# Performance work log

Measured on AMD Instinct MI355X. Metric: run time of the kernel, lower is better.

The kernel has to match this reference:

```python
import jax, jax.numpy as jnp
import numpy as np

U, I, K = 20000, 10000, 64
HID = [128, 64, 32, 16]  # hidden[0] must equal 2*K
B = 4096


def _lin(key, out_f, in_f):
    # torch nn.Linear default init ~ U(-1/sqrt(in), 1/sqrt(in)); normal/sqrt(in) is fine for a baseline
    return jax.random.normal(key, (out_f, in_f), jnp.float32) / np.sqrt(in_f)


def setup_inputs() -> dict:
    key = jax.random.key(0)
    ks = jax.random.split(key, 12)
    # near-binary implicit-feedback interaction matrix [U+1, I+1]
    interactions = (jax.random.uniform(ks[0], (U + 1, I + 1)) < 0.05).astype(jnp.float32)
    user_idx = jax.random.randint(ks[1], (B,), 0, U)
    item_idx = jax.random.randint(ks[2], (B,), 0, I)
    W_u = _lin(ks[3], K, I)   # proj_u: Linear(n_items -> K, bias=False)
    W_i = _lin(ks[4], K, U)   # proj_i: Linear(n_users -> K, bias=False)
    inp = dict(interactions=interactions, user_idx=user_idx, item_idx=item_idx,
               W_u=W_u, W_i=W_i)
    # matching_fn: 3 blocks of Linear + LayerNorm (+ReLU, dropout=0 in eval)
    for j in range(1, len(HID)):
        inp[f'W{j}'] = _lin(ks[4 + j], HID[j], HID[j - 1])
        inp[f'b{j}'] = jnp.zeros((HID[j],), jnp.float32)
        inp[f'g{j}'] = jnp.ones((HID[j],), jnp.float32)
        inp[f'be{j}'] = jnp.zeros((HID[j],), jnp.float32)
    inp['Wp'] = _lin(ks[8], 1, HID[-1])
    inp['bp'] = jnp.zeros((1,), jnp.float32)
    return inp


def _layernorm(x, g, b, eps=1e-5):
    m = jnp.mean(x, axis=-1, keepdims=True)
    v = jnp.mean(jnp.square(x - m), axis=-1, keepdims=True)
    return (x - m) * jax.lax.rsqrt(v + eps) * g + b


def reference(interactions, user_idx, item_idx, W_u, W_i,
              W1, b1, g1, be1, W2, b2, g2, be2, W3, b3, g3, be3, Wp, bp):
    rows = jnp.arange(user_idx.shape[0])
    # gather user history rows [B, I], zero-mask the target item
    u_slice = interactions[user_idx, :-1].at[rows, item_idx].set(0.0)
    # gather item history rows [B, U], zero-mask the target user
    i_slice = interactions.T[item_idx, :-1].at[rows, user_idx].set(0.0)
    u_emb = u_slice @ W_u.T  # [B, K]
    i_emb = i_slice @ W_i.T  # [B, K]
    x = jnp.concatenate([u_emb, i_emb], axis=-1)  # [B, 2K]
    for (W, b, g, be) in ((W1, b1, g1, be1), (W2, b2, g2, be2), (W3, b3, g3, be3)):
        x = jax.nn.relu(_layernorm(x @ W.T + b, g, be))
    logit = jnp.squeeze(x @ Wp.T + bp, -1)  # [B]
    return logit
```

## Files before the change

### kernel.cpp

```cpp
#include <hip/hip_runtime.h>

#define U_ROWS 20000
#define I_COLS 10000
#define LDI    10001
#define B_N    4096
#define SC     625
#define NPAN_C 79
#define NC_C   8
#define SUT    79
#define NP_U   8
#define SPU_T  10
#define SU_P   316
#define ABP    10240
#define ABRP   1280

typedef __attribute__((ext_vector_type(8))) __bf16 bf16x8;
typedef __attribute__((ext_vector_type(4))) float f32x4;

__device__ __forceinline__ unsigned short f2bf(float f) {
    unsigned int u = __float_as_uint(f);
    return (unsigned short)((u + 0x7FFFu + ((u >> 16) & 1u)) >> 16);
}

__device__ __forceinline__ bf16x8 expand8(unsigned int byte) {
    union { unsigned int i[4]; bf16x8 v; } af;
#pragma unroll
    for (int q = 0; q < 4; ++q) {
        unsigned int lo = (byte & (1u << (2 * q)))     ? 0x00003F80u : 0u;
        unsigned int hi = (byte & (1u << (2 * q + 1))) ? 0x3F800000u : 0u;
        af.i[q] = lo | hi;
    }
    return af.v;
}

__global__ __launch_bounds__(256) void k_bitize(
    const float* __restrict__ A,
    unsigned int* __restrict__ Abit, unsigned char* __restrict__ Abr,
    const float* __restrict__ Wu, const float* __restrict__ Wi,
    unsigned short* __restrict__ Pu, unsigned short* __restrict__ Pi,
    const float* __restrict__ W1, const float* __restrict__ W2, const float* __restrict__ W3,
    float* __restrict__ Wt1, float* __restrict__ Wt2, float* __restrict__ Wt3,
    float* __restrict__ WuT, float* __restrict__ WiT)
{
    const int t = threadIdx.x;
    if ((int)blockIdx.x < SC) {
        const int s = blockIdx.x;
        unsigned int wq[5][8];
#pragma unroll
        for (int q = 0; q < 5; ++q)
#pragma unroll
            for (int j = 0; j < 8; ++j) wq[q][j] = 0u;

        for (int r = 0; r < 32; ++r) {
            const float* row = A + (size_t)(s * 32 + r) * LDI;
#pragma unroll
            for (int q = 0; q < 5; ++q) {
                const int c0 = 8 * t + 2048 * q;
                f32x4 a0 = *(const f32x4*)(row + c0);
                f32x4 a1 = *(const f32x4*)(row + c0 + 4);
                unsigned int b = 0;
#pragma unroll
                for (int j = 0; j < 8; ++j) {
                    float av = (j < 4) ? a0[j] : a1[j - 4];
                    unsigned int bit = (__float_as_uint(av) >> 23) & 1u;
                    if (q == 4 && (c0 + j) >= I_COLS) bit = 0;
                    b |= bit << j;
                    wq[q][j] |= bit << r;
                }
                Abr[(size_t)(s * 32 + r) * ABRP + q * 256 + t] = (unsigned char)b;
            }
        }
        unsigned int* ob = Abit + (size_t)s * ABP;
#pragma unroll
        for (int q = 0; q < 5; ++q) {
            uint4 v0, v1;
            v0.x = wq[q][0]; v0.y = wq[q][1]; v0.z = wq[q][2]; v0.w = wq[q][3];
            v1.x = wq[q][4]; v1.y = wq[q][5]; v1.z = wq[q][6]; v1.w = wq[q][7];
            *(uint4*)(ob + 2048 * q + 8 * t)     = v0;
            *(uint4*)(ob + 2048 * q + 8 * t + 4) = v1;
        }
        return;
    }

    const int NU = SU_P * 2048, NC2 = SC * 2048;
    int idx = ((int)blockIdx.x - SC) * 256 + t;
    if (idx < NU + NC2) {
        const float* W = (idx < NU) ? Wu : Wi;
        unsigned short* out = (idx < NU) ? Pu : Pi;
        int n_k = (idx < NU) ? I_COLS : U_ROWS;
        int li = (idx < NU) ? idx : idx - NU;
        int j  = li & 7;
        int l  = (li >> 3) & 63;
        int nb = (li >> 9) & 3;
        int s  = li >> 11;
        int n  = nb * 16 + (l & 15);
        int k  = s * 32 + ((l >> 4) << 3) + j;
        float v = (k < n_k) ? W[(size_t)n * n_k + k] : 0.0f;
        out[li] = f2bf(v);
        return;
    }
    int r2 = idx - (NU + NC2);
    if (r2 < 64 * 128) { int r = r2 / 128, c = r2 % 128; Wt1[c * 64 + r] = W1[r2]; return; }
    r2 -= 64 * 128;
    if (r2 < 32 * 64)  { int r = r2 / 64,  c = r2 % 64;  Wt2[c * 32 + r] = W2[r2]; return; }
    r2 -= 32 * 64;
    if (r2 < 16 * 32)  { int r = r2 / 32,  c = r2 % 32;  Wt3[c * 16 + r] = W3[r2]; return; }
    r2 -= 16 * 32;
    if (r2 < 64 * I_COLS) {
        int n = r2 / I_COLS, k = r2 % I_COLS;
        WuT[(size_t)k * 64 + n] = Wu[r2];
        return;
    }
    r2 -= 64 * I_COLS;
    if (r2 < 64 * U_ROWS) {
        int n = r2 / U_ROWS, u = r2 % U_ROWS;
        WiT[(size_t)u * 64 + n] = Wi[r2];
        return;
    }
}

__global__ __launch_bounds__(256) void k_gemm2(
    const unsigned int* __restrict__ Abit, const unsigned char* __restrict__ Abr,
    const int* __restrict__ uidx,
    const unsigned short* __restrict__ Bpu, const unsigned short* __restrict__ Bpc,
    float* __restrict__ Upart, float* __restrict__ Cpart)
{
    const int t = threadIdx.x, lane = t & 63, w = t >> 6;
    const int rl = lane & 15, g = lane >> 4;
    const int CB = NPAN_C * NC_C;

    if ((int)blockIdx.x < CB) {
        const int p = blockIdx.x % NC_C, mb = blockIdx.x / NC_C;
        const int i0 = mb * 128;
        const int spc = (SC + NC_C - 1) / NC_C;
        const int s0 = p * spc;
        const int s1 = (SC < s0 + spc) ? SC : (s0 + spc);
        const int widx = i0 + w * 32 + rl;
        const int gsh = g * 8;

        f32x4 acc[2][4];
#pragma unroll
        for (int mt = 0; mt < 2; ++mt)
#pragma unroll
            for (int nb = 0; nb < 4; ++nb) acc[mt][nb] = (f32x4)(0.0f);

        for (int s = s0; s < s1; ++s) {
            const unsigned int* ws = Abit + (size_t)s * ABP + widx;
            unsigned int Wd0 = ws[0];
            unsigned int Wd1 = ws[16];
            bf16x8 bv[4];
#pragma unroll
            for (int nb = 0; nb < 4; ++nb)
                bv[nb] = *(const bf16x8*)(Bpc + ((size_t)(s * 4 + nb) * 64 + lane) * 8);
            bf16x8 a0 = expand8((Wd0 >> gsh) & 0xFFu);
            bf16x8 a1 = expand8((Wd1 >> gsh) & 0xFFu);
#pragma unroll
            for (int nb = 0; nb < 4; ++nb)
                acc[0][nb] = __builtin_amdgcn_mfma_f32_16x16x32_bf16(a0, bv[nb], acc[0][nb], 0, 0, 0);
#pragma unroll
            for (int nb = 0; nb < 4; ++nb)
                acc[1][nb] = __builtin_amdgcn_mfma_f32_16x16x32_bf16(a1, bv[nb], acc[1][nb], 0, 0, 0);
        }

        float* outp = Cpart + (size_t)p * I_COLS * 64;
#pragma unroll
        for (int mt = 0; mt < 2; ++mt)
#pragma unroll
            for (int nb = 0; nb < 4; ++nb)
#pragma unroll
                for (int reg = 0; reg < 4; ++reg) {
                    int i = i0 + w * 32 + mt * 16 + g * 4 + reg;
                    if (i < I_COLS) outp[(size_t)i * 64 + nb * 16 + rl] = acc[mt][nb][reg];
                }
    } else {
        const int bid = blockIdx.x - CB;
        const int p = bid % NP_U, mb = bid / NP_U;
        const int r0 = mb * 64;
        const int s0 = p * SPU_T;
        const int s1 = (SUT < s0 + SPU_T) ? SUT : (s0 + SPU_T);

        const int ur = uidx[r0 + w * 16 + rl];
        const unsigned char* ab = Abr + (size_t)ur * ABRP;

        f32x4 acc[4];
#pragma unroll
        for (int nb = 0; nb < 4; ++nb) acc[nb] = (f32x4)(0.0f);

        for (int s = s0; s < s1; ++s) {
#pragma unroll
            for (int ks = 0; ks < 4; ++ks) {
                const int kk = s * 4 + ks;
                unsigned int byte = ab[s * 16 + ks * 4 + g];
                bf16x8 afv = expand8(byte);
                bf16x8 bv[4];
#pragma unroll
                for (int nb = 0; nb < 4; ++nb)
                    bv[nb] = *(const bf16x8*)(Bpu + ((size_t)(kk * 4 + nb) * 64 + lane) * 8);
#pragma unroll
                for (int nb = 0; nb < 4; ++nb)
                    acc[nb] = __builtin_amdgcn_mfma_f32_16x16x32_bf16(afv, bv[nb], acc[nb], 0, 0, 0);
            }
        }

        float* outp = Upart + (size_t)p * B_N * 64;
#pragma unroll
        for (int nb = 0; nb < 4; ++nb)
#pragma unroll
            for (int reg = 0; reg < 4; ++reg) {
                int r = r0 + w * 16 + g * 4 + reg;
                outp[(size_t)r * 64 + nb * 16 + rl] = acc[nb][reg];
            }
    }
}

__device__ __forceinline__ float redsum64(float x) {
    x += __shfl_xor(x, 1);  x += __shfl_xor(x, 2);  x += __shfl_xor(x, 4);
    x += __shfl_xor(x, 8);  x += __shfl_xor(x, 16); x += __shfl_xor(x, 32);
    return x;
}
__device__ __forceinline__ float redsum32(float x) {
    x += __shfl_xor(x, 1); x += __shfl_xor(x, 2); x += __shfl_xor(x, 4);
    x += __shfl_xor(x, 8); x += __shfl_xor(x, 16);
    return x;
}
__device__ __forceinline__ float redsum16(float x) {
    x += __shfl_xor(x, 1); x += __shfl_xor(x, 2); x += __shfl_xor(x, 4);
    x += __shfl_xor(x, 8);
    return x;
}

__global__ __launch_bounds__(256) void k_epi(
    const float* __restrict__ A, const int* __restrict__ uidx, const int* __restrict__ iidx,
    const float* __restrict__ Upart, const float* __restrict__ Cpart, int NP, int NC,
    const float* __restrict__ WuT, const float* __restrict__ WiT,
    const float* __restrict__ Wt1, const float* __restrict__ b1, const float* __restrict__ g1, const float* __restrict__ be1,
    const float* __restrict__ Wt2, const float* __restrict__ b2, const float* __restrict__ g2, const float* __restrict__ be2,
    const float* __restrict__ Wt3, const float* __restrict__ b3, const float* __restrict__ g3, const float* __restrict__ be3,
    const float* __restrict__ Wp, const float* __restrict__ bp,
    float* __restrict__ out)
{
    const int t = threadIdx.x, lane = t & 63, w = t >> 6;
    const int r = blockIdx.x * 4 + w;
    const int u = uidx[r], it = iidx[r];
    const float a_ui = A[(size_t)u * LDI + it];

    float ue = 0.f, ie = 0.f;
    for (int p0 = 0; p0 < NP; ++p0) ue += Upart[((size_t)p0 * B_N + r) * 64 + lane];
    for (int p0 = 0; p0 < NC; ++p0) ie += Cpart[((size_t)p0 * I_COLS + it) * 64 + lane];
    ue -= a_ui * WuT[(size_t)it * 64 + lane];
    ie -= a_ui * WiT[(size_t)u * 64 + lane];

    float h = b1[lane];
    for (int c = 0; c < 64; ++c) h += __shfl(ue, c) * Wt1[c * 64 + lane];
    for (int c = 0; c < 64; ++c) h += __shfl(ie, c) * Wt1[(64 + c) * 64 + lane];
    {
        float m = redsum64(h) * (1.0f / 64.0f);
        float d = h - m;
        float v = redsum64(d * d) * (1.0f / 64.0f);
        h = d * rsqrtf(v + 1e-5f) * g1[lane] + be1[lane];
        h = fmaxf(h, 0.0f);
    }
    const int l2 = lane & 31;
    float h2 = b2[l2];
    for (int c = 0; c < 64; ++c) h2 += __shfl(h, c) * Wt2[c * 32 + l2];
    {
        float m = redsum32(h2) * (1.0f / 32.0f);
        float d = h2 - m;
        float v = redsum32(d * d) * (1.0f / 32.0f);
        h2 = d * rsqrtf(v + 1e-5f) * g2[l2] + be2[l2];
        h2 = fmaxf(h2, 0.0f);
    }
    const int l3 = lane & 15;
    float h3 = b3[l3];
    for (int c = 0; c < 32; ++c) h3 += __shfl(h2, c) * Wt3[c * 16 + l3];
    {
        float m = redsum16(h3) * (1.0f / 16.0f);
        float d = h3 - m;
        float v = redsum16(d * d) * (1.0f / 16.0f);
        h3 = d * rsqrtf(v + 1e-5f) * g3[l3] + be3[l3];
        h3 = fmaxf(h3, 0.0f);
    }
    float tt = h3 * Wp[l3];
    tt = redsum16(tt);
    if (lane == 0) out[r] = tt + bp[0];
}

extern "C" void kernel_launch(void* const* d_in, const int* in_sizes, int n_in,
                              void* d_out, int out_size, void* d_ws, size_t ws_size,
                              hipStream_t stream)
{
    const float* A    = (const float*)d_in[0];
    const int*   uidx = (const int*)d_in[1];
    const int*   iidx = (const int*)d_in[2];
    const float* W_u  = (const float*)d_in[3];
    const float* W_i  = (const float*)d_in[4];
    const float* W1   = (const float*)d_in[5];
    const float* b1   = (const float*)d_in[6];
    const float* g1   = (const float*)d_in[7];
    const float* be1  = (const float*)d_in[8];
    const float* W2   = (const float*)d_in[9];
    const float* b2   = (const float*)d_in[10];
    const float* g2   = (const float*)d_in[11];
    const float* be2  = (const float*)d_in[12];
    const float* W3   = (const float*)d_in[13];
    const float* b3   = (const float*)d_in[14];
    const float* g3   = (const float*)d_in[15];
    const float* be3  = (const float*)d_in[16];
    const float* Wp   = (const float*)d_in[17];
    const float* bp   = (const float*)d_in[18];
    float* out = (float*)d_out;

    unsigned int*  Abit = (unsigned int*)d_ws;
    unsigned char* Abr  = (unsigned char*)(Abit + (size_t)SC * ABP);
    unsigned short* Wtu_p = (unsigned short*)(Abr + (size_t)U_ROWS * ABRP);
    unsigned short* Wti_p = Wtu_p + (size_t)SU_P * 2048;
    float* Wt1 = (float*)(Wti_p + (size_t)SC * 2048);
    float* Wt2 = Wt1 + 128 * 64;
    float* Wt3 = Wt2 + 64 * 32;
    float* WuT = Wt3 + 32 * 16;
    float* WiT = WuT + (size_t)I_COLS * 64;
    float* Upart = WiT + (size_t)U_ROWS * 64;
    float* Cpart = Upart + (size_t)NP_U * B_N * 64;

    int prep_tot = (SU_P + SC) * 2048 + 64 * 128 + 32 * 64 + 16 * 32
                 + 64 * I_COLS + 64 * U_ROWS;
    int grid1 = SC + (prep_tot + 255) / 256;

    hipLaunchKernelGGL(k_bitize, dim3(grid1), dim3(256), 0, stream,
                       A, Abit, Abr, W_u, W_i, Wtu_p, Wti_p,
                       W1, W2, W3, Wt1, Wt2, Wt3, WuT, WiT);

    hipLaunchKernelGGL(k_gemm2, dim3(NPAN_C * NC_C + 64 * NP_U), dim3(256), 0, stream,
                       Abit, Abr, uidx, Wtu_p, Wti_p, Upart, Cpart);

    hipLaunchKernelGGL(k_epi, dim3(B_N / 4), dim3(256), 0, stream,
                       A, uidx, iidx, Upart, Cpart, NP_U, NC_C,
                       WuT, WiT, Wt1, b1, g1, be1, Wt2, b2, g2, be2,
                       Wt3, b3, g3, be3, Wp, bp, out);
}
```

Measured before the change: 283.2 us.

## Drop byte-row and transposed weight copies; split bitize finer; read bitplanes in user GEMM

The bitize pass is split into five times more blocks, each handling one 2048-column quarter with strided scalar loads. It no longer writes the per-row byte copy of the interaction matrix or the transposed WuT/WiT weight copies. The user-side GEMM now reads the column-packed bit words directly, extracting one bit per row with a one-step register prefetch. The epilogue reads the correction weights with strides from the original W_u/W_i. This removes tens of MB of prep writes, but each user-GEMM row now reads full 32-bit words to use a single bit, and the epilogue loads are uncoalesced.

```diff
diff --git a/kernel.cpp b/kernel.cpp
--- a/kernel.cpp
+++ b/kernel.cpp
@@ -5,14 +5,13 @@
 #define LDI    10001
 #define B_N    4096
 #define SC     625
+#define ABP    10240
 #define NPAN_C 79
 #define NC_C   8
-#define SUT    79
 #define NP_U   8
-#define SPU_T  10
+#define KKT    316
 #define SU_P   316
-#define ABP    10240
-#define ABRP   1280
+#define SQ     5
 
 typedef __attribute__((ext_vector_type(8))) __bf16 bf16x8;
 typedef __attribute__((ext_vector_type(4))) float f32x4;
@@ -34,56 +33,42 @@
 }
 
 __global__ __launch_bounds__(256) void k_bitize(
-    const float* __restrict__ A,
-    unsigned int* __restrict__ Abit, unsigned char* __restrict__ Abr,
+    const float* __restrict__ A, unsigned int* __restrict__ Abit,
     const float* __restrict__ Wu, const float* __restrict__ Wi,
     unsigned short* __restrict__ Pu, unsigned short* __restrict__ Pi,
     const float* __restrict__ W1, const float* __restrict__ W2, const float* __restrict__ W3,
-    float* __restrict__ Wt1, float* __restrict__ Wt2, float* __restrict__ Wt3,
-    float* __restrict__ WuT, float* __restrict__ WiT)
+    float* __restrict__ Wt1, float* __restrict__ Wt2, float* __restrict__ Wt3)
 {
     const int t = threadIdx.x;
-    if ((int)blockIdx.x < SC) {
-        const int s = blockIdx.x;
-        unsigned int wq[5][8];
-#pragma unroll
-        for (int q = 0; q < 5; ++q)
-#pragma unroll
-            for (int j = 0; j < 8; ++j) wq[q][j] = 0u;
+    if ((int)blockIdx.x < SC * SQ) {
+        const int s = blockIdx.x / SQ, q = blockIdx.x % SQ;
+        const float* base = A + (size_t)s * 32 * LDI + q * 2048 + t;
+        unsigned int acc[8];
+#pragma unroll
+        for (int m = 0; m < 8; ++m) acc[m] = 0u;
 
         for (int r = 0; r < 32; ++r) {
-            const float* row = A + (size_t)(s * 32 + r) * LDI;
-#pragma unroll
-            for (int q = 0; q < 5; ++q) {
-                const int c0 = 8 * t + 2048 * q;
-                f32x4 a0 = *(const f32x4*)(row + c0);
-                f32x4 a1 = *(const f32x4*)(row + c0 + 4);
-                unsigned int b = 0;
-#pragma unroll
-                for (int j = 0; j < 8; ++j) {
-                    float av = (j < 4) ? a0[j] : a1[j - 4];
-                    unsigned int bit = (__float_as_uint(av) >> 23) & 1u;
-                    if (q == 4 && (c0 + j) >= I_COLS) bit = 0;
-                    b |= bit << j;
-                    wq[q][j] |= bit << r;
-                }
-                Abr[(size_t)(s * 32 + r) * ABRP + q * 256 + t] = (unsigned char)b;
+            const float* row = base + (size_t)r * LDI;
+            float v[8];
+#pragma unroll
+            for (int m = 0; m < 8; ++m) v[m] = row[m * 256];
+#pragma unroll
+            for (int m = 0; m < 8; ++m) {
+                unsigned int bit = (__float_as_uint(v[m]) >> 23) & 1u;
+                acc[m] |= bit << r;
             }
         }
-        unsigned int* ob = Abit + (size_t)s * ABP;
-#pragma unroll
-        for (int q = 0; q < 5; ++q) {
-            uint4 v0, v1;
-            v0.x = wq[q][0]; v0.y = wq[q][1]; v0.z = wq[q][2]; v0.w = wq[q][3];
-            v1.x = wq[q][4]; v1.y = wq[q][5]; v1.z = wq[q][6]; v1.w = wq[q][7];
-            *(uint4*)(ob + 2048 * q + 8 * t)     = v0;
-            *(uint4*)(ob + 2048 * q + 8 * t + 4) = v1;
+        unsigned int* ob = Abit + (size_t)s * ABP + q * 2048 + t;
+#pragma unroll
+        for (int m = 0; m < 8; ++m) {
+            unsigned int a = (q * 2048 + m * 256 + t < I_COLS) ? acc[m] : 0u;
+            ob[m * 256] = a;
         }
         return;
     }
 
     const int NU = SU_P * 2048, NC2 = SC * 2048;
-    int idx = ((int)blockIdx.x - SC) * 256 + t;
+    int idx = ((int)blockIdx.x - SC * SQ) * 256 + t;
     if (idx < NU + NC2) {
         const float* W = (idx < NU) ? Wu : Wi;
         unsigned short* out = (idx < NU) ? Pu : Pi;
@@ -105,23 +90,10 @@
     if (r2 < 32 * 64)  { int r = r2 / 64,  c = r2 % 64;  Wt2[c * 32 + r] = W2[r2]; return; }
     r2 -= 32 * 64;
     if (r2 < 16 * 32)  { int r = r2 / 32,  c = r2 % 32;  Wt3[c * 16 + r] = W3[r2]; return; }
-    r2 -= 16 * 32;
-    if (r2 < 64 * I_COLS) {
-        int n = r2 / I_COLS, k = r2 % I_COLS;
-        WuT[(size_t)k * 64 + n] = Wu[r2];
-        return;
-    }
-    r2 -= 64 * I_COLS;
-    if (r2 < 64 * U_ROWS) {
-        int n = r2 / U_ROWS, u = r2 % U_ROWS;
-        WiT[(size_t)u * 64 + n] = Wi[r2];
-        return;
-    }
 }
 
 __global__ __launch_bounds__(256) void k_gemm2(
-    const unsigned int* __restrict__ Abit, const unsigned char* __restrict__ Abr,
-    const int* __restrict__ uidx,
+    const unsigned int* __restrict__ Abit, const int* __restrict__ uidx,
     const unsigned short* __restrict__ Bpu, const unsigned short* __restrict__ Bpc,
     float* __restrict__ Upart, float* __restrict__ Cpart)
 {
@@ -176,30 +148,41 @@
         const int bid = blockIdx.x - CB;
         const int p = bid % NP_U, mb = bid / NP_U;
         const int r0 = mb * 64;
-        const int s0 = p * SPU_T;
-        const int s1 = (SUT < s0 + SPU_T) ? SUT : (s0 + SPU_T);
+        const int spk = (KKT + NP_U - 1) / NP_U;
+        const int kk0 = p * spk;
+        const int kk1 = (KKT < kk0 + spk) ? KKT : (kk0 + spk);
 
         const int ur = uidx[r0 + w * 16 + rl];
-        const unsigned char* ab = Abr + (size_t)ur * ABRP;
+        const unsigned int* wrow = Abit + (size_t)(ur >> 5) * ABP;
+        const int bp = ur & 31;
 
         f32x4 acc[4];
 #pragma unroll
         for (int nb = 0; nb < 4; ++nb) acc[nb] = (f32x4)(0.0f);
 
-        for (int s = s0; s < s1; ++s) {
-#pragma unroll
-            for (int ks = 0; ks < 4; ++ks) {
-                const int kk = s * 4 + ks;
-                unsigned int byte = ab[s * 16 + ks * 4 + g];
-                bf16x8 afv = expand8(byte);
-                bf16x8 bv[4];
-#pragma unroll
-                for (int nb = 0; nb < 4; ++nb)
-                    bv[nb] = *(const bf16x8*)(Bpu + ((size_t)(kk * 4 + nb) * 64 + lane) * 8);
-#pragma unroll
-                for (int nb = 0; nb < 4; ++nb)
-                    acc[nb] = __builtin_amdgcn_mfma_f32_16x16x32_bf16(afv, bv[nb], acc[nb], 0, 0, 0);
+        uint4 pa0 = *(const uint4*)(wrow + kk0 * 32 + g * 8);
+        uint4 pa1 = *(const uint4*)(wrow + kk0 * 32 + g * 8 + 4);
+        for (int kk = kk0; kk < kk1; ++kk) {
+            uint4 a0 = pa0, a1 = pa1;
+            if (kk + 1 < kk1) {
+                pa0 = *(const uint4*)(wrow + (kk + 1) * 32 + g * 8);
+                pa1 = *(const uint4*)(wrow + (kk + 1) * 32 + g * 8 + 4);
             }
+            unsigned int wd[8] = {a0.x, a0.y, a0.z, a0.w, a1.x, a1.y, a1.z, a1.w};
+            union { unsigned int i[4]; bf16x8 v; } af;
+#pragma unroll
+            for (int q = 0; q < 4; ++q) {
+                unsigned int lo = ((wd[2 * q]     >> bp) & 1u) ? 0x00003F80u : 0u;
+                unsigned int hi = ((wd[2 * q + 1] >> bp) & 1u) ? 0x3F800000u : 0u;
+                af.i[q] = lo | hi;
+            }
+            bf16x8 bv[4];
+#pragma unroll
+            for (int nb = 0; nb < 4; ++nb)
+                bv[nb] = *(const bf16x8*)(Bpu + ((size_t)(kk * 4 + nb) * 64 + lane) * 8);
+#pragma unroll
+            for (int nb = 0; nb < 4; ++nb)
+                acc[nb] = __builtin_amdgcn_mfma_f32_16x16x32_bf16(af.v, bv[nb], acc[nb], 0, 0, 0);
         }
 
         float* outp = Upart + (size_t)p * B_N * 64;
@@ -231,8 +214,8 @@
 
 __global__ __launch_bounds__(256) void k_epi(
     const float* __restrict__ A, const int* __restrict__ uidx, const int* __restrict__ iidx,
-    const float* __restrict__ Upart, const float* __restrict__ Cpart, int NP, int NC,
-    const float* __restrict__ WuT, const float* __restrict__ WiT,
+    const float* __restrict__ Upart, const float* __restrict__ Cpart,
+    const float* __restrict__ Wu, const float* __restrict__ Wi,
     const float* __restrict__ Wt1, const float* __restrict__ b1, const float* __restrict__ g1, const float* __restrict__ be1,
     const float* __restrict__ Wt2, const float* __restrict__ b2, const float* __restrict__ g2, const float* __restrict__ be2,
     const float* __restrict__ Wt3, const float* __restrict__ b3, const float* __restrict__ g3, const float* __restrict__ be3,
@@ -245,10 +228,10 @@
     const float a_ui = A[(size_t)u * LDI + it];
 
     float ue = 0.f, ie = 0.f;
-    for (int p0 = 0; p0 < NP; ++p0) ue += Upart[((size_t)p0 * B_N + r) * 64 + lane];
-    for (int p0 = 0; p0 < NC; ++p0) ie += Cpart[((size_t)p0 * I_COLS + it) * 64 + lane];
-    ue -= a_ui * WuT[(size_t)it * 64 + lane];
-    ie -= a_ui * WiT[(size_t)u * 64 + lane];
+    for (int p0 = 0; p0 < NP_U; ++p0) ue += Upart[((size_t)p0 * B_N + r) * 64 + lane];
+    for (int p0 = 0; p0 < NC_C; ++p0) ie += Cpart[((size_t)p0 * I_COLS + it) * 64 + lane];
+    ue -= a_ui * Wu[(size_t)lane * I_COLS + it];
+    ie -= a_ui * Wi[(size_t)lane * U_ROWS + u];
 
     float h = b1[lane];
     for (int c = 0; c < 64; ++c) h += __shfl(ue, c) * Wt1[c * 64 + lane];
@@ -311,30 +294,26 @@
     float* out = (float*)d_out;
 
     unsigned int*  Abit = (unsigned int*)d_ws;
-    unsigned char* Abr  = (unsigned char*)(Abit + (size_t)SC * ABP);
-    unsigned short* Wtu_p = (unsigned short*)(Abr + (size_t)U_ROWS * ABRP);
+    unsigned short* Wtu_p = (unsigned short*)(Abit + (size_t)SC * ABP);
     unsigned short* Wti_p = Wtu_p + (size_t)SU_P * 2048;
     float* Wt1 = (float*)(Wti_p + (size_t)SC * 2048);
     float* Wt2 = Wt1 + 128 * 64;
     float* Wt3 = Wt2 + 64 * 32;
-    float* WuT = Wt3 + 32 * 16;
-    float* WiT = WuT + (size_t)I_COLS * 64;
-    float* Upart = WiT + (size_t)U_ROWS * 64;
+    float* Upart = Wt3 + 32 * 16;
     float* Cpart = Upart + (size_t)NP_U * B_N * 64;
 
-    int prep_tot = (SU_P + SC) * 2048 + 64 * 128 + 32 * 64 + 16 * 32
-                 + 64 * I_COLS + 64 * U_ROWS;
-    int grid1 = SC + (prep_tot + 255) / 256;
+    int prep_tot = (SU_P + SC) * 2048 + 64 * 128 + 32 * 64 + 16 * 32;
+    int grid1 = SC * SQ + (prep_tot + 255) / 256;
 
     hipLaunchKernelGGL(k_bitize, dim3(grid1), dim3(256), 0, stream,
-                       A, Abit, Abr, W_u, W_i, Wtu_p, Wti_p,
-                       W1, W2, W3, Wt1, Wt2, Wt3, WuT, WiT);
+                       A, Abit, W_u, W_i, Wtu_p, Wti_p,
+                       W1, W2, W3, Wt1, Wt2, Wt3);
 
     hipLaunchKernelGGL(k_gemm2, dim3(NPAN_C * NC_C + 64 * NP_U), dim3(256), 0, stream,
-                       Abit, Abr, uidx, Wtu_p, Wti_p, Upart, Cpart);
+                       Abit, uidx, Wtu_p, Wti_p, Upart, Cpart);
 
     hipLaunchKernelGGL(k_epi, dim3(B_N / 4), dim3(256), 0, stream,
-                       A, uidx, iidx, Upart, Cpart, NP_U, NC_C,
-                       WuT, WiT, Wt1, b1, g1, be1, Wt2, b2, g2, be2,
+                       A, uidx, iidx, Upart, Cpart, W_u, W_i,
+                       Wt1, b1, g1, be1, Wt2, b2, g2, be2,
                        Wt3, b3, g3, be3, Wp, bp, out);
 }
```

After: 251.1 us. 1.13x faster.
